# Kernel optimization log

Hardware: AMD Instinct MI355X
Metric: run time of the kernel (lower is better)

The kernel has to match this reference:

```python
import jax, jax.numpy as jnp
import numpy as np

EPS = 1e-8  # torch F.cosine_similarity eps


def _cosine_logits(emb, mem):
    # emb: [N, C], mem: [S, C] -> [N, S]
    num = emb @ mem.T
    denom = jnp.linalg.norm(emb, axis=1, keepdims=True) * jnp.linalg.norm(mem, axis=1)[None, :]
    return num / jnp.maximum(denom, EPS)


def setup_inputs() -> dict:
    key = jax.random.key(0)
    k1, k2, k3, k4 = jax.random.split(key, 4)
    N, S, C = 8192, 4096, 256
    return {
        "face": jax.random.normal(k1, (N, C), dtype=jnp.float32),
        "speech": jax.random.normal(k2, (N, C), dtype=jnp.float32),
        # init.normal_(mean=0, std=0.5)
        "speech_value_memory": 0.5 * jax.random.normal(k3, (S, C), dtype=jnp.float32),
        "face_key_memory": 0.5 * jax.random.normal(k4, (S, C), dtype=jnp.float32),
    }


def reference(face, speech, speech_value_memory, face_key_memory):
    # speech_encoder runs under torch.no_grad() -> stop_gradient; encoders abstracted as identity.
    speech_emb = jax.lax.stop_gradient(speech)
    face_emb = face

    speech_logits = _cosine_logits(speech_emb, speech_value_memory)      # [N, S]
    speech_address_log = jax.nn.log_softmax(speech_logits, axis=1)
    speech_address = jax.nn.softmax(speech_logits, axis=1)
    speech_emb_recall = speech_address @ speech_value_memory             # [N, C]

    face_logits = _cosine_logits(face_emb, face_key_memory)             # [N, S]
    face_address_log = jax.nn.log_softmax(face_logits, axis=1)
    face_address = jax.nn.softmax(face_logits, axis=1)
    face_emb_recall = face_address @ speech_value_memory                 # [N, C]

    return (speech_emb, speech_emb_recall, face_emb, face_emb_recall,
            speech_address_log, face_address_log)
```

## Files before the change

### kernel.cpp

```cpp
#include <hip/hip_runtime.h>
#include <hip/hip_bf16.h>
#include <cstdint>
#include <cstddef>

typedef __attribute__((ext_vector_type(8))) short bf16x8;
typedef __attribute__((ext_vector_type(4))) float f32x4;

static __device__ __forceinline__ unsigned short f2bf(float f) {
    union { float f; unsigned u; } v; v.f = f;
    return (unsigned short)((v.u + 0x7fffu + ((v.u >> 16) & 1u)) >> 16);
}
static __device__ __forceinline__ float bf2f(unsigned short h) {
    union { unsigned u; float f; } v; v.u = ((unsigned)h) << 16;
    return v.f;
}

#define NC 2097152
#define SC 1048576
#define NS 33554432
#define SPLITS 4

__global__ __launch_bounds__(64) void rownorm_kernel(
    const float* __restrict__ face, const float* __restrict__ speech,
    const float* __restrict__ svm, const float* __restrict__ fkm,
    unsigned short* __restrict__ face_n, unsigned short* __restrict__ speech_n,
    unsigned short* __restrict__ svm_n, unsigned short* __restrict__ fkm_n,
    float* __restrict__ out_face, float* __restrict__ out_speech,
    unsigned short* __restrict__ svmT)
{
    const int which = blockIdx.y;
    const int row   = blockIdx.x;
    if (which >= 2 && row >= 4096) return;

    const float* in; unsigned short* nrm; float* cpy = nullptr; bool tr = false;
    if (which == 0)      { in = speech; nrm = speech_n; cpy = out_speech; }
    else if (which == 1) { in = face;   nrm = face_n;   cpy = out_face; }
    else if (which == 2) { in = svm;    nrm = svm_n;    tr = true; }
    else                 { in = fkm;    nrm = fkm_n; }

    const int lane = threadIdx.x;
    const float4 v = *(const float4*)(in + (size_t)row * 256 + lane * 4);
    float ss = v.x * v.x + v.y * v.y + v.z * v.z + v.w * v.w;
    #pragma unroll
    for (int off = 32; off > 0; off >>= 1) ss += __shfl_xor(ss, off);
    const float rn = rsqrtf(ss);

    ushort4 o;
    o.x = f2bf(v.x * rn); o.y = f2bf(v.y * rn);
    o.z = f2bf(v.z * rn); o.w = f2bf(v.w * rn);
    *(ushort4*)(nrm + (size_t)row * 256 + lane * 4) = o;

    if (cpy) *(float4*)(cpy + (size_t)row * 256 + lane * 4) = v;

    if (tr) {
        const int c = lane * 4;
        svmT[(size_t)(c + 0) * 4096 + row] = f2bf(v.x);
        svmT[(size_t)(c + 1) * 4096 + row] = f2bf(v.y);
        svmT[(size_t)(c + 2) * 4096 + row] = f2bf(v.z);
        svmT[(size_t)(c + 3) * 4096 + row] = f2bf(v.w);
    }
}

__global__ __launch_bounds__(256) void gemm_logits_kernel(
    const unsigned short* __restrict__ speech_n,
    const unsigned short* __restrict__ face_n,
    const unsigned short* __restrict__ svm_n,
    const unsigned short* __restrict__ fkm_n,
    unsigned short* __restrict__ logits)
{
    __shared__ unsigned short As[128 * 32];
    __shared__ unsigned short Bs[128 * 32];
    const int side = blockIdx.z;
    const unsigned short* A = side ? face_n : speech_n;
    const unsigned short* B = side ? fkm_n  : svm_n;
    unsigned short* Lg = logits + ((size_t)side * NS);

    const int row0 = blockIdx.y * 128;
    const int col0 = blockIdx.x * 128;
    const int tid  = threadIdx.x;
    const int wave = tid >> 6, lane = tid & 63;
    const int wm = (wave >> 1) * 64, wn = (wave & 1) * 64;
    const int quad = lane >> 4, r16 = lane & 15;

    f32x4 acc[4][4];
    #pragma unroll
    for (int i = 0; i < 4; i++)
        #pragma unroll
        for (int j = 0; j < 4; j++) acc[i][j] = 0.f;

    for (int k0 = 0; k0 < 256; k0 += 32) {
        #pragma unroll
        for (int it = 0; it < 2; ++it) {
            const int c = tid + it * 256;
            const int r = c >> 2, cj = c & 3;
            *(uint4*)(&As[r * 32 + cj * 8]) =
                *(const uint4*)(A + (size_t)(row0 + r) * 256 + k0 + cj * 8);
            *(uint4*)(&Bs[r * 32 + cj * 8]) =
                *(const uint4*)(B + (size_t)(col0 + r) * 256 + k0 + cj * 8);
        }
        __syncthreads();
        bf16x8 af[4], bfr[4];
        #pragma unroll
        for (int i = 0; i < 4; i++) {
            af[i]  = *(const bf16x8*)(&As[(wm + i * 16 + r16) * 32 + quad * 8]);
            bfr[i] = *(const bf16x8*)(&Bs[(wn + i * 16 + r16) * 32 + quad * 8]);
        }
        #pragma unroll
        for (int i = 0; i < 4; i++)
            #pragma unroll
            for (int j = 0; j < 4; j++)
                acc[i][j] = __builtin_amdgcn_mfma_f32_16x16x32_bf16(
                    af[i], bfr[j], acc[i][j], 0, 0, 0);
        __syncthreads();
    }

    #pragma unroll
    for (int i = 0; i < 4; i++) {
        #pragma unroll
        for (int j = 0; j < 4; j++) {
            const int r  = row0 + wm + i * 16 + quad * 4;
            const int cc = col0 + wn + j * 16 + r16;
            #pragma unroll
            for (int rr = 0; rr < 4; rr++)
                Lg[(size_t)(r + rr) * 4096 + cc] = f2bf(acc[i][j][rr]);
        }
    }
}

__global__ __launch_bounds__(256) void softmax_kernel(
    const unsigned short* __restrict__ logits,
    unsigned short* __restrict__ P,
    float* __restrict__ out_slog, float* __restrict__ out_flog)
{
    __shared__ float red[4];
    const int b = blockIdx.x;
    const int side = b >> 13, row = b & 8191;
    const size_t off = (size_t)side * NS + ((size_t)row << 12);
    const unsigned short* lp = logits + off;
    unsigned short* pp = P + off;
    float* op = (side ? out_flog : out_slog) + ((size_t)row << 12);
    const int t = threadIdx.x;

    float x[16], e[16];
    float s = 0.f;
    #pragma unroll
    for (int i = 0; i < 2; i++) {
        const int j = t + i * 256;
        unsigned short vv[8];
        *(uint4*)vv = *(const uint4*)(lp + (size_t)j * 8);
        #pragma unroll
        for (int k = 0; k < 8; k++) {
            const float xv = bf2f(vv[k]);
            x[i * 8 + k] = xv;
            const float ev = __expf(xv);
            e[i * 8 + k] = ev;
            s += ev;
        }
    }
    #pragma unroll
    for (int o = 32; o > 0; o >>= 1) s += __shfl_xor(s, o);
    if ((t & 63) == 0) red[t >> 6] = s;
    __syncthreads();
    s = red[0] + red[1] + red[2] + red[3];
    const float lse = __logf(s);
    const float inv = 1.0f / s;

    #pragma unroll
    for (int i = 0; i < 2; i++) {
        const int j = t + i * 256;
        float4 o0, o1;
        o0.x = x[i*8+0] - lse; o0.y = x[i*8+1] - lse;
        o0.z = x[i*8+2] - lse; o0.w = x[i*8+3] - lse;
        o1.x = x[i*8+4] - lse; o1.y = x[i*8+5] - lse;
        o1.z = x[i*8+6] - lse; o1.w = x[i*8+7] - lse;
        ((float4*)op)[j * 2]     = o0;
        ((float4*)op)[j * 2 + 1] = o1;
        unsigned short pv[8];
        #pragma unroll
        for (int k = 0; k < 8; k++) pv[k] = f2bf(e[i * 8 + k] * inv);
        *(uint4*)(pp + (size_t)j * 8) = *(uint4*)pv;
    }
}

__global__ __launch_bounds__(256) void gemm_recall_kernel(
    const unsigned short* __restrict__ P,
    const unsigned short* __restrict__ BT,
    float* __restrict__ part)
{
    __shared__ unsigned short As[64 * 32];
    __shared__ unsigned short Bs[256 * 32];
    const int row0  = blockIdx.x * 64;
    const int split = blockIdx.y;
    const int side  = blockIdx.z;
    const unsigned short* A = P + (size_t)side * NS;
    float* outp = part + (((size_t)side * SPLITS + split) << 21);
    const int kbase = split * (4096 / SPLITS);

    const int tid  = threadIdx.x;
    const int wave = tid >> 6, lane = tid & 63;
    const int wn = wave * 64;
    const int quad = lane >> 4, r16 = lane & 15;

    f32x4 acc[4][4];
    #pragma unroll
    for (int i = 0; i < 4; i++)
        #pragma unroll
        for (int j = 0; j < 4; j++) acc[i][j] = 0.f;

    for (int k0 = kbase; k0 < kbase + 4096 / SPLITS; k0 += 32) {
        *(uint4*)(&As[(tid >> 2) * 32 + (tid & 3) * 8]) =
            *(const uint4*)(A + (size_t)(row0 + (tid >> 2)) * 4096 + k0 + (tid & 3) * 8);
        #pragma unroll
        for (int it = 0; it < 4; ++it) {
            const int c = tid + it * 256, r = c >> 2, cj = c & 3;
            *(uint4*)(&Bs[r * 32 + cj * 8]) =
                *(const uint4*)(BT + (size_t)r * 4096 + k0 + cj * 8);
        }
        __syncthreads();
        bf16x8 af[4], bfr[4];
        #pragma unroll
        for (int i = 0; i < 4; i++) {
            af[i]  = *(const bf16x8*)(&As[(i * 16 + r16) * 32 + quad * 8]);
            bfr[i] = *(const bf16x8*)(&Bs[(wn + i * 16 + r16) * 32 + quad * 8]);
        }
        #pragma unroll
        for (int i = 0; i < 4; i++)
            #pragma unroll
            for (int j = 0; j < 4; j++)
                acc[i][j] = __builtin_amdgcn_mfma_f32_16x16x32_bf16(
                    af[i], bfr[j], acc[i][j], 0, 0, 0);
        __syncthreads();
    }

    #pragma unroll
    for (int i = 0; i < 4; i++) {
        #pragma unroll
        for (int j = 0; j < 4; j++) {
            const int r  = row0 + i * 16 + quad * 4;
            const int cc = wn + j * 16 + r16;
            #pragma unroll
            for (int rr = 0; rr < 4; rr++)
                outp[(size_t)(r + rr) * 256 + cc] = acc[i][j][rr];
        }
    }
}

__global__ __launch_bounds__(256) void reduce_kernel(
    const float* __restrict__ part,
    float* __restrict__ out_srecall, float* __restrict__ out_frecall)
{
    const int idx = blockIdx.x * 256 + threadIdx.x;
    const int side = idx >> 19;
    const int off = idx & ((1 << 19) - 1);
    const float4* p = (const float4*)(part + ((size_t)side * SPLITS << 21));
    float4 s = p[off];
    #pragma unroll
    for (int sp = 1; sp < SPLITS; sp++) {
        const float4 v = p[off + (size_t)sp * (1 << 19)];
        s.x += v.x; s.y += v.y; s.z += v.z; s.w += v.w;
    }
    float4* o = (float4*)(side ? out_frecall : out_srecall);
    o[off] = s;
}

extern "C" void kernel_launch(void* const* d_in, const int* in_sizes, int n_in,
                              void* d_out, int out_size, void* d_ws, size_t ws_size,
                              hipStream_t stream) {
    const float* face   = (const float*)d_in[0];
    const float* speech = (const float*)d_in[1];
    const float* svm    = (const float*)d_in[2];
    const float* fkm    = (const float*)d_in[3];

    const int N = 8192, S = 4096, C = 256;
    float* out = (float*)d_out;
    float* out_speech  = out;
    float* out_srecall = out + (size_t)N * C;
    float* out_face    = out + 2 * (size_t)N * C;
    float* out_frecall = out + 3 * (size_t)N * C;
    float* out_slog    = out + 4 * (size_t)N * C;
    float* out_flog    = out_slog + (size_t)N * S;

    unsigned short* wsu = (unsigned short*)d_ws;
    unsigned short* speech_n = wsu;
    unsigned short* face_n   = speech_n + NC;
    unsigned short* svm_n    = face_n + NC;
    unsigned short* fkm_n    = svm_n + SC;
    unsigned short* svmT     = fkm_n + SC;
    unsigned short* logits   = svmT + SC;
    unsigned short* Pws      = logits + 2 * (size_t)NS;
    float* part = (float*)(Pws + 2 * (size_t)NS);

    dim3 g1(N, 4);
    rownorm_kernel<<<g1, 64, 0, stream>>>(face, speech, svm, fkm,
                                          face_n, speech_n, svm_n, fkm_n,
                                          out_face, out_speech, svmT);

    dim3 g2(S / 128, N / 128, 2);
    gemm_logits_kernel<<<g2, 256, 0, stream>>>(speech_n, face_n, svm_n, fkm_n, logits);

    softmax_kernel<<<2 * N, 256, 0, stream>>>(logits, Pws, out_slog, out_flog);

    dim3 g4(N / 64, SPLITS, 2);
    gemm_recall_kernel<<<g4, 256, 0, stream>>>(Pws, svmT, part);

    reduce_kernel<<<2 * (N * C / 4) / 256, 256, 0, stream>>>(part, out_srecall, out_frecall);
}
```

Before: 543.4 us.

## Fuse softmax exp into recall GEMM, drop P buffer and split-K reduce

The softmax kernel now writes only log-probs (as nontemporal stores) plus a per-row LSE. The recall GEMM recomputes the probabilities on the fly from the bf16 logits as exp(x - lse), which removes the bf16 P buffer write and its reread. Split-K partials are accumulated straight into the zeroed outputs with atomic adds, so the separate reduce kernel is gone; the rownorm kernel gains an extra grid slice that zeroes those outputs. Both GEMMs load tiles with global_load_lds direct-to-LDS transfers, and the logits GEMM stages its epilogue through LDS so stores are coalesced. The cost is extra exp work inside the GEMM and float atomics whose summation order is nondeterministic.

Result: faster. 524.9 us (-3.4%).

```diff
diff --git a/kernel.cpp b/kernel.cpp
--- a/kernel.cpp
+++ b/kernel.cpp
@@ -13,6 +13,12 @@
 static __device__ __forceinline__ float bf2f(unsigned short h) {
     union { unsigned u; float f; } v; v.u = ((unsigned)h) << 16;
     return v.f;
+}
+
+static __device__ __forceinline__ void gld_lds16(const unsigned short* g, unsigned short* l) {
+    __builtin_amdgcn_global_load_lds(
+        (const __attribute__((address_space(1))) void*)g,
+        (__attribute__((address_space(3))) void*)l, 16, 0, 0);
 }
 
 #define NC 2097152
@@ -26,10 +32,19 @@
     unsigned short* __restrict__ face_n, unsigned short* __restrict__ speech_n,
     unsigned short* __restrict__ svm_n, unsigned short* __restrict__ fkm_n,
     float* __restrict__ out_face, float* __restrict__ out_speech,
-    unsigned short* __restrict__ svmT)
+    unsigned short* __restrict__ svmT,
+    float* __restrict__ out_srecall, float* __restrict__ out_frecall)
 {
     const int which = blockIdx.y;
     const int row   = blockIdx.x;
+    const int lane  = threadIdx.x;
+
+    if (which == 4) {
+        const float4 z = make_float4(0.f, 0.f, 0.f, 0.f);
+        *(float4*)(out_srecall + (size_t)row * 256 + lane * 4) = z;
+        *(float4*)(out_frecall + (size_t)row * 256 + lane * 4) = z;
+        return;
+    }
     if (which >= 2 && row >= 4096) return;
 
     const float* in; unsigned short* nrm; float* cpy = nullptr; bool tr = false;
@@ -38,7 +53,6 @@
     else if (which == 2) { in = svm;    nrm = svm_n;    tr = true; }
     else                 { in = fkm;    nrm = fkm_n; }
 
-    const int lane = threadIdx.x;
     const float4 v = *(const float4*)(in + (size_t)row * 256 + lane * 4);
     float ss = v.x * v.x + v.y * v.y + v.z * v.z + v.w * v.w;
     #pragma unroll
@@ -68,8 +82,9 @@
     const unsigned short* __restrict__ fkm_n,
     unsigned short* __restrict__ logits)
 {
-    __shared__ unsigned short As[128 * 32];
-    __shared__ unsigned short Bs[128 * 32];
+    __shared__ unsigned short smem[128 * 32 * 2];
+    unsigned short* As = smem;
+    unsigned short* Bs = smem + 128 * 32;
     const int side = blockIdx.z;
     const unsigned short* A = side ? face_n : speech_n;
     const unsigned short* B = side ? fkm_n  : svm_n;
@@ -82,6 +97,9 @@
     const int wm = (wave >> 1) * 64, wn = (wave & 1) * 64;
     const int quad = lane >> 4, r16 = lane & 15;
 
+    const int r0 = tid >> 2,          cj0 = tid & 3;
+    const int r1 = (tid + 256) >> 2,  cj1 = (tid + 256) & 3;
+
     f32x4 acc[4][4];
     #pragma unroll
     for (int i = 0; i < 4; i++)
@@ -89,16 +107,12 @@
         for (int j = 0; j < 4; j++) acc[i][j] = 0.f;
 
     for (int k0 = 0; k0 < 256; k0 += 32) {
-        #pragma unroll
-        for (int it = 0; it < 2; ++it) {
-            const int c = tid + it * 256;
-            const int r = c >> 2, cj = c & 3;
-            *(uint4*)(&As[r * 32 + cj * 8]) =
-                *(const uint4*)(A + (size_t)(row0 + r) * 256 + k0 + cj * 8);
-            *(uint4*)(&Bs[r * 32 + cj * 8]) =
-                *(const uint4*)(B + (size_t)(col0 + r) * 256 + k0 + cj * 8);
-        }
-        __syncthreads();
+        gld_lds16(A + (size_t)(row0 + r0) * 256 + k0 + cj0 * 8, As + (size_t)(wave * 64) * 8);
+        gld_lds16(B + (size_t)(col0 + r0) * 256 + k0 + cj0 * 8, Bs + (size_t)(wave * 64) * 8);
+        gld_lds16(A + (size_t)(row0 + r1) * 256 + k0 + cj1 * 8, As + (size_t)(256 + wave * 64) * 8);
+        gld_lds16(B + (size_t)(col0 + r1) * 256 + k0 + cj1 * 8, Bs + (size_t)(256 + wave * 64) * 8);
+        __syncthreads();
+
         bf16x8 af[4], bfr[4];
         #pragma unroll
         for (int i = 0; i < 4; i++) {
@@ -114,22 +128,32 @@
         __syncthreads();
     }
 
-    #pragma unroll
-    for (int i = 0; i < 4; i++) {
-        #pragma unroll
-        for (int j = 0; j < 4; j++) {
-            const int r  = row0 + wm + i * 16 + quad * 4;
-            const int cc = col0 + wn + j * 16 + r16;
+    unsigned short* tb = smem + wave * 2048;
+    #pragma unroll
+    for (int h = 0; h < 2; ++h) {
+        #pragma unroll
+        for (int i2 = 0; i2 < 2; ++i2)
             #pragma unroll
-            for (int rr = 0; rr < 4; rr++)
-                Lg[(size_t)(r + rr) * 4096 + cc] = f2bf(acc[i][j][rr]);
-        }
+            for (int j = 0; j < 4; ++j)
+                #pragma unroll
+                for (int rr = 0; rr < 4; ++rr)
+                    tb[(i2 * 16 + quad * 4 + rr) * 64 + j * 16 + r16] =
+                        f2bf(acc[2 * h + i2][j][rr]);
+        __syncthreads();
+        #pragma unroll
+        for (int p = 0; p < 4; ++p) {
+            const int lrow = p * 8 + (lane >> 3);
+            const int lcol = (lane & 7) * 8;
+            const uint4 v = *(const uint4*)(tb + lrow * 64 + lcol);
+            *(uint4*)(Lg + (size_t)(row0 + wm + h * 32 + lrow) * 4096 + col0 + wn + lcol) = v;
+        }
+        __syncthreads();
     }
 }
 
 __global__ __launch_bounds__(256) void softmax_kernel(
     const unsigned short* __restrict__ logits,
-    unsigned short* __restrict__ P,
+    float* __restrict__ lse_ws,
     float* __restrict__ out_slog, float* __restrict__ out_flog)
 {
     __shared__ float red[4];
@@ -137,11 +161,10 @@
     const int side = b >> 13, row = b & 8191;
     const size_t off = (size_t)side * NS + ((size_t)row << 12);
     const unsigned short* lp = logits + off;
-    unsigned short* pp = P + off;
     float* op = (side ? out_flog : out_slog) + ((size_t)row << 12);
     const int t = threadIdx.x;
 
-    float x[16], e[16];
+    float x[16];
     float s = 0.f;
     #pragma unroll
     for (int i = 0; i < 2; i++) {
@@ -152,9 +175,7 @@
         for (int k = 0; k < 8; k++) {
             const float xv = bf2f(vv[k]);
             x[i * 8 + k] = xv;
-            const float ev = __expf(xv);
-            e[i * 8 + k] = ev;
-            s += ev;
+            s += __expf(xv);
         }
     }
     #pragma unroll
@@ -163,43 +184,42 @@
     __syncthreads();
     s = red[0] + red[1] + red[2] + red[3];
     const float lse = __logf(s);
-    const float inv = 1.0f / s;
+    if (t == 0) lse_ws[(size_t)side * 8192 + row] = lse;
 
     #pragma unroll
     for (int i = 0; i < 2; i++) {
         const int j = t + i * 256;
-        float4 o0, o1;
-        o0.x = x[i*8+0] - lse; o0.y = x[i*8+1] - lse;
-        o0.z = x[i*8+2] - lse; o0.w = x[i*8+3] - lse;
-        o1.x = x[i*8+4] - lse; o1.y = x[i*8+5] - lse;
-        o1.z = x[i*8+6] - lse; o1.w = x[i*8+7] - lse;
-        ((float4*)op)[j * 2]     = o0;
-        ((float4*)op)[j * 2 + 1] = o1;
-        unsigned short pv[8];
-        #pragma unroll
-        for (int k = 0; k < 8; k++) pv[k] = f2bf(e[i * 8 + k] * inv);
-        *(uint4*)(pp + (size_t)j * 8) = *(uint4*)pv;
+        f32x4 o0, o1;
+        o0[0] = x[i*8+0] - lse; o0[1] = x[i*8+1] - lse;
+        o0[2] = x[i*8+2] - lse; o0[3] = x[i*8+3] - lse;
+        o1[0] = x[i*8+4] - lse; o1[1] = x[i*8+5] - lse;
+        o1[2] = x[i*8+6] - lse; o1[3] = x[i*8+7] - lse;
+        __builtin_nontemporal_store(o0, (f32x4*)op + j * 2);
+        __builtin_nontemporal_store(o1, (f32x4*)op + j * 2 + 1);
     }
 }
 
 __global__ __launch_bounds__(256) void gemm_recall_kernel(
-    const unsigned short* __restrict__ P,
+    const unsigned short* __restrict__ logits,
+    const float* __restrict__ lse,
     const unsigned short* __restrict__ BT,
-    float* __restrict__ part)
+    float* __restrict__ out_srecall, float* __restrict__ out_frecall)
 {
     __shared__ unsigned short As[64 * 32];
     __shared__ unsigned short Bs[256 * 32];
     const int row0  = blockIdx.x * 64;
     const int split = blockIdx.y;
     const int side  = blockIdx.z;
-    const unsigned short* A = P + (size_t)side * NS;
-    float* outp = part + (((size_t)side * SPLITS + split) << 21);
+    const unsigned short* A = logits + (size_t)side * NS;
+    float* outp = side ? out_frecall : out_srecall;
     const int kbase = split * (4096 / SPLITS);
 
     const int tid  = threadIdx.x;
     const int wave = tid >> 6, lane = tid & 63;
     const int wn = wave * 64;
     const int quad = lane >> 4, r16 = lane & 15;
+    const int arow = tid >> 2, acj = tid & 3;
+    const float myl = lse[(size_t)side * 8192 + row0 + arow];
 
     f32x4 acc[4][4];
     #pragma unroll
@@ -208,15 +228,20 @@
         for (int j = 0; j < 4; j++) acc[i][j] = 0.f;
 
     for (int k0 = kbase; k0 < kbase + 4096 / SPLITS; k0 += 32) {
-        *(uint4*)(&As[(tid >> 2) * 32 + (tid & 3) * 8]) =
-            *(const uint4*)(A + (size_t)(row0 + (tid >> 2)) * 4096 + k0 + (tid & 3) * 8);
+        unsigned short vv[8];
+        *(uint4*)vv = *(const uint4*)(A + (size_t)(row0 + arow) * 4096 + k0 + acj * 8);
         #pragma unroll
         for (int it = 0; it < 4; ++it) {
             const int c = tid + it * 256, r = c >> 2, cj = c & 3;
-            *(uint4*)(&Bs[r * 32 + cj * 8]) =
-                *(const uint4*)(BT + (size_t)r * 4096 + k0 + cj * 8);
-        }
-        __syncthreads();
+            gld_lds16(BT + (size_t)r * 4096 + k0 + cj * 8,
+                      Bs + (size_t)(it * 256 + wave * 64) * 8);
+        }
+        unsigned short pv[8];
+        #pragma unroll
+        for (int k = 0; k < 8; k++) pv[k] = f2bf(__expf(bf2f(vv[k]) - myl));
+        *(uint4*)(&As[arow * 32 + acj * 8]) = *(uint4*)pv;
+        __syncthreads();
+
         bf16x8 af[4], bfr[4];
         #pragma unroll
         for (int i = 0; i < 4; i++) {
@@ -240,27 +265,9 @@
             const int cc = wn + j * 16 + r16;
             #pragma unroll
             for (int rr = 0; rr < 4; rr++)
-                outp[(size_t)(r + rr) * 256 + cc] = acc[i][j][rr];
-        }
-    }
-}
-
-__global__ __launch_bounds__(256) void reduce_kernel(
-    const float* __restrict__ part,
-    float* __restrict__ out_srecall, float* __restrict__ out_frecall)
-{
-    const int idx = blockIdx.x * 256 + threadIdx.x;
-    const int side = idx >> 19;
-    const int off = idx & ((1 << 19) - 1);
-    const float4* p = (const float4*)(part + ((size_t)side * SPLITS << 21));
-    float4 s = p[off];
-    #pragma unroll
-    for (int sp = 1; sp < SPLITS; sp++) {
-        const float4 v = p[off + (size_t)sp * (1 << 19)];
-        s.x += v.x; s.y += v.y; s.z += v.z; s.w += v.w;
-    }
-    float4* o = (float4*)(side ? out_frecall : out_srecall);
-    o[off] = s;
+                unsafeAtomicAdd(&outp[(size_t)(r + rr) * 256 + cc], acc[i][j][rr]);
+        }
+    }
 }
 
 extern "C" void kernel_launch(void* const* d_in, const int* in_sizes, int n_in,
@@ -287,21 +294,20 @@
     unsigned short* fkm_n    = svm_n + SC;
     unsigned short* svmT     = fkm_n + SC;
     unsigned short* logits   = svmT + SC;
-    unsigned short* Pws      = logits + 2 * (size_t)NS;
-    float* part = (float*)(Pws + 2 * (size_t)NS);
-
-    dim3 g1(N, 4);
+    float* lse = (float*)(logits + 2 * (size_t)NS);
+
+    dim3 g1(N, 5);
     rownorm_kernel<<<g1, 64, 0, stream>>>(face, speech, svm, fkm,
                                           face_n, speech_n, svm_n, fkm_n,
-                                          out_face, out_speech, svmT);
+                                          out_face, out_speech, svmT,
+                                          out_srecall, out_frecall);
 
     dim3 g2(S / 128, N / 128, 2);
     gemm_logits_kernel<<<g2, 256, 0, stream>>>(speech_n, face_n, svm_n, fkm_n, logits);
 
-    softmax_kernel<<<2 * N, 256, 0, stream>>>(logits, Pws, out_slog, out_flog);
+    softmax_kernel<<<2 * N, 256, 0, stream>>>(logits, lse, out_slog, out_flog);
 
     dim3 g4(N / 64, SPLITS, 2);
-    gemm_recall_kernel<<<g4, 256, 0, stream>>>(Pws, svmT, part);
-
-    reduce_kernel<<<2 * (N * C / 4) / 256, 256, 0, stream>>>(part, out_srecall, out_frecall);
-}
+    gemm_recall_kernel<<<g4, 256, 0, stream>>>(logits, lse, svmT,
+                                               out_srecall, out_frecall);
+}
```
